# Optimization experiments

Measured on AMD Instinct MI355X. Metric: run time of the kernel, lower is better.

## Reference

```python
import jax, jax.numpy as jnp
import numpy as np

SIM_T = 32  # simulation_length


def uniform_spikes(rates, T):
    """Faithful port of to_uniform_spikes, vectorized over all T cycles.
    rates: (B, D) in [0,1] -> spike train (T, B, D) of {0,1} floats."""
    N = jnp.round(rates * T).astype(jnp.int32)          # (B, D)
    cycles = jnp.arange(T, dtype=jnp.float32)[:, None, None]  # (T,1,1)
    N_safe = jnp.maximum(N, 1)
    spacing = T / N_safe.astype(jnp.float32)
    mask = (N != 0) & (N != T)                          # cycle < T always holds here
    res = mask & (jnp.floor(cycles / spacing) < N_safe) & (jnp.floor(jnp.mod(cycles, spacing)) == 0)
    res = res.astype(jnp.float32)
    res = jnp.where(N == T, jnp.float32(1.0), res)      # result[N == T] = 1.0
    return res


def lif_core(spikes_in, weight, threshold):
    """LIF integration: memb += inp @ W.T; fired = threshold < memb; Default reset.
    spikes_in: (T, B, in); weight: (out, in). Returns (T, B, out) spike train."""
    B = spikes_in.shape[1]
    out_dim = weight.shape[0]

    def step(memb, s):
        memb = memb + s @ weight.T
        fired = threshold < memb                        # thresholding_mode '<'
        memb = jnp.where(fired, memb - threshold, memb) # firing_mode 'Default'
        return memb, fired.astype(jnp.float32)

    _, out_train = jax.lax.scan(step, jnp.zeros((B, out_dim), spikes_in.dtype), spikes_in)
    return out_train


def setup_inputs() -> dict:
    key = jax.random.key(0)
    k = jax.random.split(key, 8)
    B, D_in = 64, 4096
    x = jax.random.uniform(k[0], (B, D_in), dtype=jnp.float32)          # rates in [0,1]
    w0 = jax.random.normal(k[1], (4096, 4096), dtype=jnp.float32) / np.sqrt(4096.0)
    t0 = jnp.float32(1.0)
    w2 = jax.random.normal(k[2], (1000, 1024), dtype=jnp.float32) / np.sqrt(1024.0)
    t2 = jnp.float32(1.0)
    idx0 = jax.random.permutation(k[3], 4096).astype(jnp.int32)
    idx1 = jax.random.permutation(k[4], 4096).astype(jnp.int32)
    idx2 = jax.random.permutation(k[5], 1024).astype(jnp.int32)
    idx_out = jnp.arange(1000, dtype=jnp.int32)
    return {"x": x, "w0": w0, "t0": t0, "w2": w2, "t2": t2,
            "idx0": idx0, "idx1": idx1, "idx2": idx2, "idx_out": idx_out}


def reference(x, w0, t0, w2, t2, idx0, idx1, idx2, idx_out):
    B = x.shape[0]
    T = SIM_T
    # Input encoding (Uniform spike mode), train shape (T, B, 4096)
    inp_train = uniform_spikes(x, T)
    # NeuralCore 0: per-source gather + LIF
    s0 = lif_core(inp_train[:, :, idx0], w0, t0)        # (T, B, 4096)
    # ComputeOp avg_pool2d: sync barrier -> rates over full window
    rates = s0[:, :, idx1].mean(axis=0)                 # (B, 4096)
    C, H, W = 64, 8, 8
    xr = rates.reshape(B, C, H, W)
    pooled = xr.reshape(B, C, H // 2, 2, W // 2, 2).mean(axis=(3, 5))  # (B, 64, 4, 4)
    y_rates = jnp.clip(pooled.reshape(B, -1), 0.0, 1.0) # (B, 1024)
    s1 = uniform_spikes(y_rates, T)                     # (T, B, 1024)
    # NeuralCore 2
    s2 = lif_core(s1[:, :, idx2], w2, t2)               # (T, B, 1000)
    # Output accumulation over cycles (spike counts)
    return s2[:, :, idx_out].sum(axis=0)                # (B, 1000)
```

## Files before the change

### kernel.cpp

```cpp
#include <hip/hip_runtime.h>
#include <stdint.h>
#include <stddef.h>

#define D0 4096
#define D1 1024
#define NOUT 1000
#define NB 64

constexpr uint32_t spike_pattern_ct(int N) {
  if (N <= 0) return 0u;
  if (N >= 32) return 0xFFFFFFFFu;
  float sp = 32.0f / (float)N;
  uint32_t m = 0;
  for (int c = 0; c < 32; ++c) {
    double q = (double)c / (double)sp;
    int n = (int)q;
    double r = (double)c - (double)n * (double)sp;
    if (r < 1.0) m |= (1u << c);
  }
  return m;
}

__global__ void transpose_w0_k(const float* __restrict__ w, float* __restrict__ wt) {
  __shared__ float tile[32][33];
  int j0 = blockIdx.x * 32;
  int o0 = blockIdx.y * 32;
  int tx = threadIdx.x, ty = threadIdx.y;
  float4 v = *reinterpret_cast<const float4*>(&w[(size_t)(o0 + ty) * D0 + j0 + 4 * tx]);
  tile[ty][4 * tx + 0] = v.x;
  tile[ty][4 * tx + 1] = v.y;
  tile[ty][4 * tx + 2] = v.z;
  tile[ty][4 * tx + 3] = v.w;
  __syncthreads();
  float4 u;
  u.x = tile[4 * tx + 0][ty];
  u.y = tile[4 * tx + 1][ty];
  u.z = tile[4 * tx + 2][ty];
  u.w = tile[4 * tx + 3][ty];
  *reinterpret_cast<float4*>(&wt[(size_t)(j0 + ty) * D0 + o0 + 4 * tx]) = u;
}

__global__ void transpose_w2_k(const float* __restrict__ w, float* __restrict__ wt) {
  __shared__ float tile[32][33];
  int j0 = blockIdx.x * 32;
  int o0 = blockIdx.y * 32;
  int tx = threadIdx.x, ty = threadIdx.y;
  int o = o0 + ty;
  float4 v = make_float4(0.f, 0.f, 0.f, 0.f);
  if (o < NOUT) v = *reinterpret_cast<const float4*>(&w[(size_t)o * D1 + j0 + 4 * tx]);
  tile[ty][4 * tx + 0] = v.x;
  tile[ty][4 * tx + 1] = v.y;
  tile[ty][4 * tx + 2] = v.z;
  tile[ty][4 * tx + 3] = v.w;
  __syncthreads();
  float4 u;
  u.x = tile[4 * tx + 0][ty];
  u.y = tile[4 * tx + 1][ty];
  u.z = tile[4 * tx + 2][ty];
  u.w = tile[4 * tx + 3][ty];
  *reinterpret_cast<float4*>(&wt[(size_t)(j0 + ty) * D1 + o0 + 4 * tx]) = u;
}

__global__ void prep_sort0_k(const float* __restrict__ x, const int* __restrict__ idx0,
                             uint16_t* __restrict__ perm, int* __restrict__ starts) {
  __shared__ int keys[D0];
  __shared__ int hist[33];
  __shared__ int base[34];
  __shared__ int cursor[33];
  int b = blockIdx.x;
  int tid = threadIdx.x;
  if (tid < 33) hist[tid] = 0;
  __syncthreads();
  for (int j = tid; j < D0; j += 256) {
    int k = (int)rintf(x[b * D0 + idx0[j]] * 32.0f);
    keys[j] = k;
    atomicAdd(&hist[k], 1);
  }
  __syncthreads();
  if (tid == 0) {
    int s = 0;
    for (int k = 0; k < 33; ++k) { base[k] = s; cursor[k] = s; s += hist[k]; }
    base[33] = s;
  }
  __syncthreads();
  if (tid < 34) starts[b * 34 + tid] = base[tid];
  for (int j = tid; j < D0; j += 256) {
    int k = keys[j];
    int pos = atomicAdd(&cursor[k], 1);
    perm[b * D0 + pos] = (uint16_t)j;
  }
}

__global__ void prep_sort1_k(const int* __restrict__ k0, const int* __restrict__ idx1,
                             const int* __restrict__ idx2,
                             uint16_t* __restrict__ perm, int* __restrict__ starts) {
  __shared__ int keys[D1];
  __shared__ int hist[33];
  __shared__ int base[34];
  __shared__ int cursor[33];
  int b = blockIdx.x;
  int tid = threadIdx.x;
  if (tid < 33) hist[tid] = 0;
  __syncthreads();
  for (int j = tid; j < D1; j += 256) {
    int q2 = idx2[j];
    int c = q2 >> 4;
    int h2 = (q2 >> 2) & 3;
    int w2 = q2 & 3;
    int cnt = 0;
#pragma unroll
    for (int dh = 0; dh < 2; ++dh)
#pragma unroll
      for (int dw = 0; dw < 2; ++dw) {
        int q = c * 64 + (2 * h2 + dh) * 8 + (2 * w2 + dw);
        cnt += k0[b * D0 + idx1[q]];
      }
    int k = (int)rintf((float)cnt * 0.25f);
    keys[j] = k;
    atomicAdd(&hist[k], 1);
  }
  __syncthreads();
  if (tid == 0) {
    int s = 0;
    for (int k = 0; k < 33; ++k) { base[k] = s; cursor[k] = s; s += hist[k]; }
    base[33] = s;
  }
  __syncthreads();
  if (tid < 34) starts[b * 34 + tid] = base[tid];
  for (int j = tid; j < D1; j += 256) {
    int k = keys[j];
    int pos = atomicAdd(&cursor[k], 1);
    perm[b * D1 + pos] = (uint16_t)j;
  }
}

template <int D, int OSTRIDE, int TILES>
__launch_bounds__(512, 4)
__global__ void lif_core_k(const float* __restrict__ wt, const uint16_t* __restrict__ perm,
                           const int* __restrict__ starts, const float* __restrict__ thr_p,
                           int* __restrict__ cnt_out) {
  __shared__ double cshare[16][256];
  __shared__ uint16_t permS[D];
  int tid = threadIdx.x;
  int b = blockIdx.y;
  int col = tid & 255;
  int half = __builtin_amdgcn_readfirstlane(tid >> 8);

  {
    const ushort2* p2 = reinterpret_cast<const ushort2*>(perm + (size_t)b * D);
    ushort2* s2 = reinterpret_cast<ushort2*>(permS);
    for (int i = tid; i < D / 2; i += 512) s2[i] = p2[i];
  }
  __syncthreads();

  const int* st = starts + b * 34;
  double th = (double)thr_p[0];

  for (int zt = 0; zt < TILES; ++zt) {
    int o = (blockIdx.x + gridDim.x * zt) * 256 + col;

    double bs[33];
#pragma unroll
    for (int k = 1; k <= 32; ++k) bs[k] = 0.0;

#pragma unroll
    for (int k = 1; k <= 32; ++k) {
      int s = __builtin_amdgcn_readfirstlane(st[k]);
      int e = __builtin_amdgcn_readfirstlane(st[k + 1]);
      if (s == e) continue;
      int mid = s + ((e - s) >> 1);
      int i  = half ? mid : s;
      int i1 = half ? e : mid;
      double a0 = 0.0, a1 = 0.0, a2 = 0.0, a3 = 0.0;
      for (; i + 8 <= i1; i += 8) {
        int j0 = __builtin_amdgcn_readfirstlane((int)permS[i + 0]);
        int j1 = __builtin_amdgcn_readfirstlane((int)permS[i + 1]);
        int j2 = __builtin_amdgcn_readfirstlane((int)permS[i + 2]);
        int j3 = __builtin_amdgcn_readfirstlane((int)permS[i + 3]);
        int j4 = __builtin_amdgcn_readfirstlane((int)permS[i + 4]);
        int j5 = __builtin_amdgcn_readfirstlane((int)permS[i + 5]);
        int j6 = __builtin_amdgcn_readfirstlane((int)permS[i + 6]);
        int j7 = __builtin_amdgcn_readfirstlane((int)permS[i + 7]);
        float f0 = wt[(size_t)(uint32_t)j0 * OSTRIDE + o];
        float f1 = wt[(size_t)(uint32_t)j1 * OSTRIDE + o];
        float f2 = wt[(size_t)(uint32_t)j2 * OSTRIDE + o];
        float f3 = wt[(size_t)(uint32_t)j3 * OSTRIDE + o];
        float f4 = wt[(size_t)(uint32_t)j4 * OSTRIDE + o];
        float f5 = wt[(size_t)(uint32_t)j5 * OSTRIDE + o];
        float f6 = wt[(size_t)(uint32_t)j6 * OSTRIDE + o];
        float f7 = wt[(size_t)(uint32_t)j7 * OSTRIDE + o];
        a0 += (double)f0; a1 += (double)f1; a2 += (double)f2; a3 += (double)f3;
        a0 += (double)f4; a1 += (double)f5; a2 += (double)f6; a3 += (double)f7;
      }
      for (; i < i1; ++i) {
        int j = __builtin_amdgcn_readfirstlane((int)permS[i]);
        a0 += (double)wt[(size_t)(uint32_t)j * OSTRIDE + o];
      }
      bs[k] = (a0 + a1) + (a2 + a3);
    }

    __syncthreads();
    if (half) {
#pragma unroll
      for (int k = 1; k <= 16; ++k) cshare[k - 1][col] = bs[k];
    }
    __syncthreads();
    if (!half) {
#pragma unroll
      for (int k = 1; k <= 16; ++k) bs[k] += cshare[k - 1][col];
    }
    __syncthreads();
    if (half) {
#pragma unroll
      for (int k = 17; k <= 32; ++k) cshare[k - 17][col] = bs[k];
    }
    __syncthreads();
    if (!half) {
#pragma unroll
      for (int k = 17; k <= 32; ++k) bs[k] += cshare[k - 17][col];

      double memb = 0.0;
      int cnt = 0;
#pragma unroll
      for (int t = 0; t < 32; ++t) {
#pragma unroll
        for (int k = 1; k <= 32; ++k)
          if ((spike_pattern_ct(k) >> t) & 1u) memb += bs[k];
        if (memb > th) { memb -= th; ++cnt; }
      }
      cnt_out[(size_t)b * OSTRIDE + o] = cnt;
    }
  }
}

__global__ void write_out_k(const int* __restrict__ cnt2, const int* __restrict__ idx_out,
                            float* __restrict__ out) {
  int i = blockIdx.x * 256 + threadIdx.x;
  if (i >= NB * NOUT) return;
  int b = i / NOUT;
  int r = i - b * NOUT;
  out[i] = (float)cnt2[b * D1 + idx_out[r]];
}

extern "C" void kernel_launch(void* const* d_in, const int* in_sizes, int n_in,
                              void* d_out, int out_size, void* d_ws, size_t ws_size,
                              hipStream_t stream) {
  const float* x      = (const float*)d_in[0];
  const float* w0     = (const float*)d_in[1];
  const float* t0     = (const float*)d_in[2];
  const float* w2     = (const float*)d_in[3];
  const float* t2     = (const float*)d_in[4];
  const int*   idx0   = (const int*)d_in[5];
  const int*   idx1   = (const int*)d_in[6];
  const int*   idx2   = (const int*)d_in[7];
  const int*   idx_out= (const int*)d_in[8];
  float* out = (float*)d_out;

  char* ws = (char*)d_ws;
  float*    w0T    = (float*)ws;    ws += (size_t)D0 * D0 * 4;
  float*    w2T    = (float*)ws;    ws += (size_t)D1 * D1 * 4;
  uint16_t* perm0  = (uint16_t*)ws; ws += (size_t)NB * D0 * 2;
  uint16_t* perm2  = (uint16_t*)ws; ws += (size_t)NB * D1 * 2;
  int*      k0     = (int*)ws;      ws += (size_t)NB * D0 * 4;
  int*      cnt2   = (int*)ws;      ws += (size_t)NB * D1 * 4;
  int*      starts0= (int*)ws;      ws += (size_t)NB * 34 * 4;
  int*      starts2= (int*)ws;      ws += (size_t)NB * 34 * 4;

  transpose_w0_k<<<dim3(D0 / 32, D0 / 32), dim3(8, 32), 0, stream>>>(w0, w0T);
  transpose_w2_k<<<dim3(D1 / 32, D1 / 32), dim3(8, 32), 0, stream>>>(w2, w2T);
  prep_sort0_k<<<NB, 256, 0, stream>>>(x, idx0, perm0, starts0);
  lif_core_k<D0, D0, 2><<<dim3(8, NB, 1), 512, 0, stream>>>(w0T, perm0, starts0, t0, k0);
  prep_sort1_k<<<NB, 256, 0, stream>>>(k0, idx1, idx2, perm2, starts2);
  lif_core_k<D1, D1, 1><<<dim3(4, NB, 1), 512, 0, stream>>>(w2T, perm2, starts2, t2, cnt2);
  write_out_k<<<(NB * NOUT + 255) / 256, 256, 0, stream>>>(cnt2, idx_out, out);
}
```

Baseline: 432.6 us.

## Pad sorted buckets to 8, read packed indices, double-buffer weight gathers

The bucket sort now pads each rate bucket to a multiple of 8 entries and also stores the bucket lengths. The LIF kernel reads indices as packed 32-bit pairs from shared memory, which means fewer LDS reads and readfirstlane ops. The gather loop is software-pipelined with two register sets so the next group's weight loads are in flight while the previous group accumulates. Launch bounds drop to 2 blocks per CU, giving more registers for the double buffer at the cost of occupancy. Padding also enlarges the perm arrays and adds a zero-fill pass in the prep kernels.

```diff
diff --git a/kernel.cpp b/kernel.cpp
--- a/kernel.cpp
+++ b/kernel.cpp
@@ -6,6 +6,8 @@
 #define D1 1024
 #define NOUT 1000
 #define NB 64
+#define PD0 4352
+#define PD1 1264
 
 constexpr uint32_t spike_pattern_ct(int N) {
   if (N <= 0) return 0u;
@@ -70,6 +72,7 @@
   int b = blockIdx.x;
   int tid = threadIdx.x;
   if (tid < 33) hist[tid] = 0;
+  for (int p = tid; p < PD0; p += 256) perm[(size_t)b * PD0 + p] = 0;
   __syncthreads();
   for (int j = tid; j < D0; j += 256) {
     int k = (int)rintf(x[b * D0 + idx0[j]] * 32.0f);
@@ -79,15 +82,19 @@
   __syncthreads();
   if (tid == 0) {
     int s = 0;
-    for (int k = 0; k < 33; ++k) { base[k] = s; cursor[k] = s; s += hist[k]; }
+    for (int k = 0; k < 33; ++k) {
+      base[k] = s; cursor[k] = s;
+      s = (s + hist[k] + 7) & ~7;
+    }
     base[33] = s;
   }
   __syncthreads();
-  if (tid < 34) starts[b * 34 + tid] = base[tid];
+  if (tid < 34) starts[b * 68 + tid] = base[tid];
+  if (tid < 33) starts[b * 68 + 34 + tid] = hist[tid];
   for (int j = tid; j < D0; j += 256) {
     int k = keys[j];
     int pos = atomicAdd(&cursor[k], 1);
-    perm[b * D0 + pos] = (uint16_t)j;
+    perm[(size_t)b * PD0 + pos] = (uint16_t)j;
   }
 }
 
@@ -101,6 +108,7 @@
   int b = blockIdx.x;
   int tid = threadIdx.x;
   if (tid < 33) hist[tid] = 0;
+  for (int p = tid; p < PD1; p += 256) perm[(size_t)b * PD1 + p] = 0;
   __syncthreads();
   for (int j = tid; j < D1; j += 256) {
     int q2 = idx2[j];
@@ -122,39 +130,74 @@
   __syncthreads();
   if (tid == 0) {
     int s = 0;
-    for (int k = 0; k < 33; ++k) { base[k] = s; cursor[k] = s; s += hist[k]; }
+    for (int k = 0; k < 33; ++k) {
+      base[k] = s; cursor[k] = s;
+      s = (s + hist[k] + 7) & ~7;
+    }
     base[33] = s;
   }
   __syncthreads();
-  if (tid < 34) starts[b * 34 + tid] = base[tid];
+  if (tid < 34) starts[b * 68 + tid] = base[tid];
+  if (tid < 33) starts[b * 68 + 34 + tid] = hist[tid];
   for (int j = tid; j < D1; j += 256) {
     int k = keys[j];
     int pos = atomicAdd(&cursor[k], 1);
-    perm[b * D1 + pos] = (uint16_t)j;
-  }
-}
-
-template <int D, int OSTRIDE, int TILES>
-__launch_bounds__(512, 4)
+    perm[(size_t)b * PD1 + pos] = (uint16_t)j;
+  }
+}
+
+template <int D, int PD, int OSTRIDE, int TILES>
+__launch_bounds__(512, 2)
 __global__ void lif_core_k(const float* __restrict__ wt, const uint16_t* __restrict__ perm,
                            const int* __restrict__ starts, const float* __restrict__ thr_p,
                            int* __restrict__ cnt_out) {
   __shared__ double cshare[16][256];
-  __shared__ uint16_t permS[D];
+  __shared__ uint16_t permS[PD];
   int tid = threadIdx.x;
   int b = blockIdx.y;
   int col = tid & 255;
   int half = __builtin_amdgcn_readfirstlane(tid >> 8);
 
   {
-    const ushort2* p2 = reinterpret_cast<const ushort2*>(perm + (size_t)b * D);
+    const ushort2* p2 = reinterpret_cast<const ushort2*>(perm + (size_t)b * PD);
     ushort2* s2 = reinterpret_cast<ushort2*>(permS);
-    for (int i = tid; i < D / 2; i += 512) s2[i] = p2[i];
-  }
-  __syncthreads();
-
-  const int* st = starts + b * 34;
+    for (int i = tid; i < PD / 2; i += 512) s2[i] = p2[i];
+  }
+  __syncthreads();
+
+  const int* stA = starts + b * 68;
+  const int* stL = starts + b * 68 + 34;
   double th = (double)thr_p[0];
+
+#define RDIDX(P) do { \
+    const uint32_t* _q = reinterpret_cast<const uint32_t*>(permS + ip); \
+    uint32_t _w0 = _q[0], _w1 = _q[1], _w2 = _q[2], _w3 = _q[3]; \
+    uint32_t _s0 = __builtin_amdgcn_readfirstlane(_w0); \
+    uint32_t _s1 = __builtin_amdgcn_readfirstlane(_w1); \
+    uint32_t _s2 = __builtin_amdgcn_readfirstlane(_w2); \
+    uint32_t _s3 = __builtin_amdgcn_readfirstlane(_w3); \
+    P##0 = _s0 & 0xffffu; P##1 = _s0 >> 16; \
+    P##2 = _s1 & 0xffffu; P##3 = _s1 >> 16; \
+    P##4 = _s2 & 0xffffu; P##5 = _s2 >> 16; \
+    P##6 = _s3 & 0xffffu; P##7 = _s3 >> 16; \
+    ip += 8; \
+  } while (0)
+
+#define GATHER(F, P) do { \
+    F##0 = wt[(size_t)P##0 * OSTRIDE + o]; \
+    F##1 = wt[(size_t)P##1 * OSTRIDE + o]; \
+    F##2 = wt[(size_t)P##2 * OSTRIDE + o]; \
+    F##3 = wt[(size_t)P##3 * OSTRIDE + o]; \
+    F##4 = wt[(size_t)P##4 * OSTRIDE + o]; \
+    F##5 = wt[(size_t)P##5 * OSTRIDE + o]; \
+    F##6 = wt[(size_t)P##6 * OSTRIDE + o]; \
+    F##7 = wt[(size_t)P##7 * OSTRIDE + o]; \
+  } while (0)
+
+#define ACC8(F) do { \
+    a0 += (double)F##0; a1 += (double)F##1; a2 += (double)F##2; a3 += (double)F##3; \
+    a0 += (double)F##4; a1 += (double)F##5; a2 += (double)F##6; a3 += (double)F##7; \
+  } while (0)
 
   for (int zt = 0; zt < TILES; ++zt) {
     int o = (blockIdx.x + gridDim.x * zt) * 256 + col;
@@ -165,36 +208,46 @@
 
 #pragma unroll
     for (int k = 1; k <= 32; ++k) {
-      int s = __builtin_amdgcn_readfirstlane(st[k]);
-      int e = __builtin_amdgcn_readfirstlane(st[k + 1]);
-      if (s == e) continue;
-      int mid = s + ((e - s) >> 1);
-      int i  = half ? mid : s;
-      int i1 = half ? e : mid;
+      int hs0 = __builtin_amdgcn_readfirstlane(stA[k]);
+      int len = __builtin_amdgcn_readfirstlane(stL[k]);
+      if (len == 0) continue;
+      int half_lo = ((len >> 1) + 7) & ~7;
+      int mid8 = half_lo < len ? half_lo : len;
+      int ip  = half ? hs0 + mid8 : hs0;
+      int myn = half ? len - mid8 : mid8;
+      if (myn == 0) continue;
+      int ng = myn >> 3, rem = myn & 7;
+      uint32_t pA0, pA1, pA2, pA3, pA4, pA5, pA6, pA7;
+      uint32_t pB0, pB1, pB2, pB3, pB4, pB5, pB6, pB7;
+      float fA0, fA1, fA2, fA3, fA4, fA5, fA6, fA7;
+      float fB0, fB1, fB2, fB3, fB4, fB5, fB6, fB7;
       double a0 = 0.0, a1 = 0.0, a2 = 0.0, a3 = 0.0;
-      for (; i + 8 <= i1; i += 8) {
-        int j0 = __builtin_amdgcn_readfirstlane((int)permS[i + 0]);
-        int j1 = __builtin_amdgcn_readfirstlane((int)permS[i + 1]);
-        int j2 = __builtin_amdgcn_readfirstlane((int)permS[i + 2]);
-        int j3 = __builtin_amdgcn_readfirstlane((int)permS[i + 3]);
-        int j4 = __builtin_amdgcn_readfirstlane((int)permS[i + 4]);
-        int j5 = __builtin_amdgcn_readfirstlane((int)permS[i + 5]);
-        int j6 = __builtin_amdgcn_readfirstlane((int)permS[i + 6]);
-        int j7 = __builtin_amdgcn_readfirstlane((int)permS[i + 7]);
-        float f0 = wt[(size_t)(uint32_t)j0 * OSTRIDE + o];
-        float f1 = wt[(size_t)(uint32_t)j1 * OSTRIDE + o];
-        float f2 = wt[(size_t)(uint32_t)j2 * OSTRIDE + o];
-        float f3 = wt[(size_t)(uint32_t)j3 * OSTRIDE + o];
-        float f4 = wt[(size_t)(uint32_t)j4 * OSTRIDE + o];
-        float f5 = wt[(size_t)(uint32_t)j5 * OSTRIDE + o];
-        float f6 = wt[(size_t)(uint32_t)j6 * OSTRIDE + o];
-        float f7 = wt[(size_t)(uint32_t)j7 * OSTRIDE + o];
-        a0 += (double)f0; a1 += (double)f1; a2 += (double)f2; a3 += (double)f3;
-        a0 += (double)f4; a1 += (double)f5; a2 += (double)f6; a3 += (double)f7;
+      if (ng > 0) {
+        RDIDX(pA); GATHER(fA, pA);
+        int g = 1;
+        for (; g + 1 < ng; g += 2) {
+          RDIDX(pB); GATHER(fB, pB);
+          ACC8(fA);
+          RDIDX(pA); GATHER(fA, pA);
+          ACC8(fB);
+        }
+        if (g < ng) {
+          RDIDX(pB); GATHER(fB, pB);
+          ACC8(fA);
+          ACC8(fB);
+        } else {
+          ACC8(fA);
+        }
       }
-      for (; i < i1; ++i) {
-        int j = __builtin_amdgcn_readfirstlane((int)permS[i]);
-        a0 += (double)wt[(size_t)(uint32_t)j * OSTRIDE + o];
+      if (rem) {
+        RDIDX(pA); GATHER(fA, pA);
+        a0 += (double)fA0;
+        if (rem > 1) a1 += (double)fA1;
+        if (rem > 2) a2 += (double)fA2;
+        if (rem > 3) a3 += (double)fA3;
+        if (rem > 4) a0 += (double)fA4;
+        if (rem > 5) a1 += (double)fA5;
+        if (rem > 6) a2 += (double)fA6;
       }
       bs[k] = (a0 + a1) + (a2 + a3);
     }
@@ -231,6 +284,9 @@
       cnt_out[(size_t)b * OSTRIDE + o] = cnt;
     }
   }
+#undef RDIDX
+#undef GATHER
+#undef ACC8
 }
 
 __global__ void write_out_k(const int* __restrict__ cnt2, const int* __restrict__ idx_out,
@@ -259,18 +315,18 @@
   char* ws = (char*)d_ws;
   float*    w0T    = (float*)ws;    ws += (size_t)D0 * D0 * 4;
   float*    w2T    = (float*)ws;    ws += (size_t)D1 * D1 * 4;
-  uint16_t* perm0  = (uint16_t*)ws; ws += (size_t)NB * D0 * 2;
-  uint16_t* perm2  = (uint16_t*)ws; ws += (size_t)NB * D1 * 2;
+  uint16_t* perm0  = (uint16_t*)ws; ws += (size_t)NB * PD0 * 2;
+  uint16_t* perm2  = (uint16_t*)ws; ws += (size_t)NB * PD1 * 2;
   int*      k0     = (int*)ws;      ws += (size_t)NB * D0 * 4;
   int*      cnt2   = (int*)ws;      ws += (size_t)NB * D1 * 4;
-  int*      starts0= (int*)ws;      ws += (size_t)NB * 34 * 4;
-  int*      starts2= (int*)ws;      ws += (size_t)NB * 34 * 4;
+  int*      starts0= (int*)ws;      ws += (size_t)NB * 68 * 4;
+  int*      starts2= (int*)ws;      ws += (size_t)NB * 68 * 4;
 
   transpose_w0_k<<<dim3(D0 / 32, D0 / 32), dim3(8, 32), 0, stream>>>(w0, w0T);
   transpose_w2_k<<<dim3(D1 / 32, D1 / 32), dim3(8, 32), 0, stream>>>(w2, w2T);
   prep_sort0_k<<<NB, 256, 0, stream>>>(x, idx0, perm0, starts0);
-  lif_core_k<D0, D0, 2><<<dim3(8, NB, 1), 512, 0, stream>>>(w0T, perm0, starts0, t0, k0);
+  lif_core_k<D0, PD0, D0, 2><<<dim3(8, NB, 1), 512, 0, stream>>>(w0T, perm0, starts0, t0, k0);
   prep_sort1_k<<<NB, 256, 0, stream>>>(k0, idx1, idx2, perm2, starts2);
-  lif_core_k<D1, D1, 1><<<dim3(4, NB, 1), 512, 0, stream>>>(w2T, perm2, starts2, t2, cnt2);
+  lif_core_k<D1, PD1, D1, 1><<<dim3(4, NB, 1), 512, 0, stream>>>(w2T, perm2, starts2, t2, cnt2);
   write_out_k<<<(NB * NOUT + 255) / 256, 256, 0, stream>>>(cnt2, idx_out, out);
 }
```

Result: faster. 384.9 us (-11.0%).
